# Optimization experiments

Hardware: AMD Instinct MI355X
Metric: run time of the kernel (lower is better)

Reference implementation:

```python
import jax, jax.numpy as jnp
import numpy as np

B, S, C, H, W = 8, 32, 3, 256, 256


def setup_inputs() -> dict:
    key = jax.random.key(0)
    k1, k2 = jax.random.split(key)
    return {
        "input": jax.random.normal(k1, (B, S, C, H, W), dtype=jnp.float32),
        "target": jax.random.normal(k2, (B, C, H, W), dtype=jnp.float32),
    }


def _l2norm(x, axis):
    # F.normalize: x / max(||x||_2, eps)
    return x / jnp.maximum(jnp.linalg.norm(x, axis=axis, keepdims=True), 1e-12)


def _forward(input, target):
    b, s, c, h, w = input.shape
    # target: [B,C,H,W] -> permute(0,1,3,2) -> [B,C,W,H] -> flatten(1,2) -> [B, C*W, H]
    target_f = _l2norm(jnp.transpose(target, (0, 1, 3, 2)).reshape(b, c * w, h), axis=1)
    # input: [B,S,C,H,W] -> permute(0,1,2,4,3) -> [B,S,C,W,H] -> flatten(2,3) -> [B,S,C*W,H]
    input_f = _l2norm(jnp.transpose(input, (0, 1, 2, 4, 3)).reshape(b, s, c * w, h), axis=2)

    def corr_one(xf, wf):
        # xf: [S, C*W, H] as conv batch, wf: [C*W, H] as single-output-channel kernel
        y = jax.lax.conv_general_dilated(
            xf, wf[None], window_strides=(1,), padding=[(h - 1, h - 1)],
            dimension_numbers=("NCH", "OIH", "NCH"))
        return y[:, 0, :h]  # first H shift positions (overlap sizes 1..H)

    corr = jax.vmap(corr_one)(input_f, target_f)  # [B, S, H]
    corr = corr / jnp.arange(1, h + 1, dtype=input.dtype)  # mean over overlap size

    overlap = jnp.argmax(corr, axis=-1)            # [B, S] best overlap per sample
    shift = (h - 1) - overlap                      # rows to shift up by

    # out[b,s,:,r,:] = input[b,s,:,r+shift,:] for r < overlap, else 0
    h_idx = jnp.arange(h)[None, None, :] + shift[:, :, None]  # [B, S, H]
    valid = h_idx < h
    idx = jnp.clip(h_idx, 0, h - 1)[:, :, None, :, None]      # [B,S,1,H,1]
    gathered = jnp.take_along_axis(input, idx, axis=3)
    return jnp.where(valid[:, :, None, :, None], gathered, jnp.zeros((), input.dtype))


def reference(input, target):
    return _forward(input, target)
```

## Files before the change

### kernel.cpp

```cpp
#include <hip/hip_runtime.h>

#define B_ 8
#define S_ 32
#define C_ 3
#define H_ 256
#define W_ 256
#define HW_ (H_*W_)
#define CHW_ (C_*H_*W_)
#define NINROWS (B_*S_*H_)
#define NTGROWS (B_*H_)

typedef __attribute__((ext_vector_type(8))) short bf16x8;
typedef __attribute__((ext_vector_type(4))) float f32x4;

__device__ __forceinline__ ushort f2bf(float x) {
  unsigned u = __float_as_uint(x);
  return (ushort)((u + 0x7FFFu + ((u >> 16) & 1u)) >> 16);
}
__device__ __forceinline__ float bf2f(ushort h) {
  return __uint_as_float(((unsigned)h) << 16);
}

__global__ void ct_norms(const float* __restrict__ input,
                         const float* __restrict__ target,
                         float* __restrict__ nin, float* __restrict__ ntg) {
  int gw = (int)((blockIdx.x * (size_t)blockDim.x + threadIdx.x) >> 6);
  int lane = threadIdx.x & 63;
  const float* base;
  if (gw < NINROWS) {
    int h = gw & (H_-1);
    int bs = gw >> 8;
    base = input + (size_t)bs * CHW_ + (size_t)h * W_;
  } else {
    int r = gw - NINROWS;
    int h = r & (H_-1);
    int b = r >> 8;
    base = target + (size_t)b * CHW_ + (size_t)h * W_;
  }
  float ss = 0.f;
#pragma unroll
  for (int c = 0; c < C_; ++c)
#pragma unroll
    for (int tt = 0; tt < W_/64; ++tt) {
      float v = base[c*HW_ + tt*64 + lane];
      ss = fmaf(v, v, ss);
    }
#pragma unroll
  for (int off = 32; off; off >>= 1) ss += __shfl_xor(ss, off);
  if (lane == 0) {
    float n = fmaxf(sqrtf(ss), 1e-12f);
    if (gw < NINROWS) nin[gw] = n;
    else ntg[gw - NINROWS] = n;
  }
}

__global__ __launch_bounds__(512)
void ct_corr_mfma(const float* __restrict__ input,
                  const float* __restrict__ target,
                  const float* __restrict__ nin,
                  const float* __restrict__ ntg,
                  int* __restrict__ shift_out) {
  __shared__ ushort Ah[8192], Al[8192], Bh[8192], Bl[8192];
  __shared__ float nin_s[256], ntg_s[256], corrS[256];
  __shared__ unsigned long long wkey[4];

  const int bs = blockIdx.x;
  const int b  = bs >> 5;
  const int t  = threadIdx.x;
  const int lane = t & 63;
  const int wid  = t >> 6;
  const int wm   = wid >> 2;
  const int wn   = wid & 3;

  const float* Abase = input  + (size_t)bs * CHW_;
  const float* Tbase = target + (size_t)b  * CHW_;

  if (t < 256) {
    nin_s[t] = nin[bs*256 + t];
    ntg_s[t] = ntg[b*256 + t];
    corrS[t] = 0.f;
  }

  f32x4 acc[8][4];
#pragma unroll
  for (int m = 0; m < 8; ++m)
#pragma unroll
    for (int n = 0; n < 4; ++n) acc[m][n] = (f32x4){0.f, 0.f, 0.f, 0.f};

  float4 pa[4], pb[4];

  auto issue = [&](int kt) {
    const float* Ab = Abase + (size_t)(kt >> 3) * HW_ + (kt & 7) * 32;
    const float* Tb = Tbase + (size_t)(kt >> 3) * HW_ + (kt & 7) * 32;
#pragma unroll
    for (int p = 0; p < 4; ++p) {
      int f   = p * 512 + t;
      int row = (f >> 7) * 16 + ((f >> 1) & 15);
      int kk  = ((f >> 5) & 3) * 8 + (f & 1) * 4;
      pa[p] = *(const float4*)(Ab + (size_t)row * W_ + kk);
      pb[p] = *(const float4*)(Tb + (size_t)row * W_ + kk);
    }
  };

  auto stash = [&]() {
#pragma unroll
    for (int p = 0; p < 4; ++p) {
      int f   = p * 512 + t;
      int idx = (f >> 7) * 512 + ((f >> 5) & 3) * 128 + ((f >> 1) & 15) * 8 + (f & 1) * 4;
      float4 va = pa[p], vb = pb[p];
      ushort4 hv, lv;
      hv.x = f2bf(va.x); lv.x = f2bf(va.x - bf2f(hv.x));
      hv.y = f2bf(va.y); lv.y = f2bf(va.y - bf2f(hv.y));
      hv.z = f2bf(va.z); lv.z = f2bf(va.z - bf2f(hv.z));
      hv.w = f2bf(va.w); lv.w = f2bf(va.w - bf2f(hv.w));
      *(ushort4*)&Ah[idx] = hv;
      *(ushort4*)&Al[idx] = lv;
      hv.x = f2bf(vb.x); lv.x = f2bf(vb.x - bf2f(hv.x));
      hv.y = f2bf(vb.y); lv.y = f2bf(vb.y - bf2f(hv.y));
      hv.z = f2bf(vb.z); lv.z = f2bf(vb.z - bf2f(hv.z));
      hv.w = f2bf(vb.w); lv.w = f2bf(vb.w - bf2f(hv.w));
      *(ushort4*)&Bh[idx] = hv;
      *(ushort4*)&Bl[idx] = lv;
    }
  };

  issue(0);
  for (int kt = 0; kt < 24; ++kt) {
    __syncthreads();
    stash();
    __syncthreads();
    if (kt < 23) issue(kt + 1);

    bf16x8 bh[4], bl[4];
#pragma unroll
    for (int n = 0; n < 4; ++n) {
      int ct = wn * 4 + n;
      bh[n] = *(const bf16x8*)&Bh[ct * 512 + lane * 8];
      bl[n] = *(const bf16x8*)&Bl[ct * 512 + lane * 8];
    }
#pragma unroll
    for (int m = 0; m < 8; ++m) {
      int rt = wm * 8 + m;
      bf16x8 ah = *(const bf16x8*)&Ah[rt * 512 + lane * 8];
      bf16x8 al = *(const bf16x8*)&Al[rt * 512 + lane * 8];
#pragma unroll
      for (int n = 0; n < 4; ++n) {
        acc[m][n] = __builtin_amdgcn_mfma_f32_16x16x32_bf16(ah, bh[n], acc[m][n], 0, 0, 0);
        acc[m][n] = __builtin_amdgcn_mfma_f32_16x16x32_bf16(ah, bl[n], acc[m][n], 0, 0, 0);
        acc[m][n] = __builtin_amdgcn_mfma_f32_16x16x32_bf16(al, bh[n], acc[m][n], 0, 0, 0);
      }
    }
  }

#pragma unroll
  for (int n = 0; n < 4; ++n) {
    int col = wn * 64 + n * 16 + (lane & 15);
    float rc = 1.0f / ntg_s[col];
#pragma unroll
    for (int m = 0; m < 8; ++m) {
      f32x4 a = acc[m][n];
#pragma unroll
      for (int r = 0; r < 4; ++r) {
        int row = wm * 128 + m * 16 + (lane >> 4) * 4 + r;
        int q = col - row;
        if (q >= 0) atomicAdd(&corrS[q], a[r] * (1.0f / nin_s[row]) * rc);
      }
    }
  }
  __syncthreads();

  if (t < 256) {
    int q = 255 - t;
    float v = corrS[q] / (float)(256 - q);
    unsigned u = __float_as_uint(v);
    u = (u & 0x80000000u) ? ~u : (u | 0x80000000u);
    unsigned long long key = ((unsigned long long)u << 32) | (unsigned)q;
#pragma unroll
    for (int off = 32; off; off >>= 1) {
      unsigned long long o = __shfl_xor(key, off);
      if (o > key) key = o;
    }
    if ((t & 63) == 0) wkey[t >> 6] = key;
  }
  __syncthreads();
  if (t == 0) {
    unsigned long long k = wkey[0];
#pragma unroll
    for (int i = 1; i < 4; ++i) if (wkey[i] > k) k = wkey[i];
    shift_out[bs] = (int)(k & 0xFFFFFFFFull);
  }
}

__global__ void ct_gather(const float* __restrict__ input,
                          const int* __restrict__ shift,
                          float* __restrict__ out) {
  size_t idx = (size_t)blockIdx.x * blockDim.x + threadIdx.x;
  int w4 = (int)(idx & 63);
  int h  = (int)((idx >> 6) & 255);
  int sc = (int)(idx >> 14);
  int bs = sc / 3;
  int hh = h + shift[bs];
  float4 v = make_float4(0.f, 0.f, 0.f, 0.f);
  if (hh < H_) v = *(const float4*)(input + ((size_t)sc << 16) + (size_t)hh * W_ + w4*4);
  *(float4*)(out + (idx << 2)) = v;
}

extern "C" void kernel_launch(void* const* d_in, const int* in_sizes, int n_in,
                              void* d_out, int out_size, void* d_ws, size_t ws_size,
                              hipStream_t stream) {
  const float* input  = (const float*)d_in[0];
  const float* target = (const float*)d_in[1];
  float* out  = (float*)d_out;
  float* nin  = (float*)d_ws;
  float* ntg  = nin + NINROWS;
  int*  shift = (int*)(ntg + NTGROWS);

  ct_norms     <<<(NINROWS + NTGROWS) / 4, 256, 0, stream>>>(input, target, nin, ntg);
  ct_corr_mfma <<<B_ * S_, 512, 0, stream>>>(input, target, nin, ntg, shift);
  ct_gather    <<<(B_*S_*C_*H_*W_/4) / 256, 256, 0, stream>>>(input, shift, out);
}
```

Baseline: 190.8 us.

## Fuse row-norm computation into correlation kernel and double-buffer LDS tiles

Drops the separate norm kernel and instead accumulates per-row sums of squares from the tiles already loaded for the MFMA correlation, reducing them in shared memory at the end. This avoids a full extra read of input and target. LDS staging is double-buffered so each tile is converted while the previous one is multiplied, leaving one barrier per iteration. The bf16 hi/lo split now truncates instead of rounding, which slightly changes precision, and the doubled LDS footprint may limit occupancy.

```diff
diff --git a/kernel.cpp b/kernel.cpp
--- a/kernel.cpp
+++ b/kernel.cpp
@@ -7,61 +7,25 @@
 #define W_ 256
 #define HW_ (H_*W_)
 #define CHW_ (C_*H_*W_)
-#define NINROWS (B_*S_*H_)
-#define NTGROWS (B_*H_)
 
 typedef __attribute__((ext_vector_type(8))) short bf16x8;
 typedef __attribute__((ext_vector_type(4))) float f32x4;
 
-__device__ __forceinline__ ushort f2bf(float x) {
-  unsigned u = __float_as_uint(x);
-  return (ushort)((u + 0x7FFFu + ((u >> 16) & 1u)) >> 16);
-}
-__device__ __forceinline__ float bf2f(ushort h) {
-  return __uint_as_float(((unsigned)h) << 16);
-}
-
-__global__ void ct_norms(const float* __restrict__ input,
-                         const float* __restrict__ target,
-                         float* __restrict__ nin, float* __restrict__ ntg) {
-  int gw = (int)((blockIdx.x * (size_t)blockDim.x + threadIdx.x) >> 6);
-  int lane = threadIdx.x & 63;
-  const float* base;
-  if (gw < NINROWS) {
-    int h = gw & (H_-1);
-    int bs = gw >> 8;
-    base = input + (size_t)bs * CHW_ + (size_t)h * W_;
-  } else {
-    int r = gw - NINROWS;
-    int h = r & (H_-1);
-    int b = r >> 8;
-    base = target + (size_t)b * CHW_ + (size_t)h * W_;
-  }
-  float ss = 0.f;
-#pragma unroll
-  for (int c = 0; c < C_; ++c)
-#pragma unroll
-    for (int tt = 0; tt < W_/64; ++tt) {
-      float v = base[c*HW_ + tt*64 + lane];
-      ss = fmaf(v, v, ss);
-    }
-#pragma unroll
-  for (int off = 32; off; off >>= 1) ss += __shfl_xor(ss, off);
-  if (lane == 0) {
-    float n = fmaxf(sqrtf(ss), 1e-12f);
-    if (gw < NINROWS) nin[gw] = n;
-    else ntg[gw - NINROWS] = n;
-  }
+__device__ __forceinline__ void split2(float x, float y, unsigned &hp, unsigned &lp) {
+  unsigned ux = __float_as_uint(x), uy = __float_as_uint(y);
+  unsigned hx = ux & 0xFFFF0000u, hy = uy & 0xFFFF0000u;
+  float lx = x - __uint_as_float(hx);
+  float ly = y - __uint_as_float(hy);
+  hp = (ux >> 16) | hy;
+  lp = (__float_as_uint(lx) >> 16) | (__float_as_uint(ly) & 0xFFFF0000u);
 }
 
 __global__ __launch_bounds__(512)
 void ct_corr_mfma(const float* __restrict__ input,
                   const float* __restrict__ target,
-                  const float* __restrict__ nin,
-                  const float* __restrict__ ntg,
                   int* __restrict__ shift_out) {
-  __shared__ ushort Ah[8192], Al[8192], Bh[8192], Bl[8192];
-  __shared__ float nin_s[256], ntg_s[256], corrS[256];
+  __shared__ ushort Ah[2][8192], Al[2][8192], Bh[2][8192], Bl[2][8192];
+  __shared__ float ninSq[256], ntgSq[256], rnin[256], rntg[256], corrS[256];
   __shared__ unsigned long long wkey[4];
 
   const int bs = blockIdx.x;
@@ -75,11 +39,7 @@
   const float* Abase = input  + (size_t)bs * CHW_;
   const float* Tbase = target + (size_t)b  * CHW_;
 
-  if (t < 256) {
-    nin_s[t] = nin[bs*256 + t];
-    ntg_s[t] = ntg[b*256 + t];
-    corrS[t] = 0.f;
-  }
+  if (t < 256) { ninSq[t] = 0.f; ntgSq[t] = 0.f; corrS[t] = 0.f; }
 
   f32x4 acc[8][4];
 #pragma unroll
@@ -88,6 +48,8 @@
     for (int n = 0; n < 4; ++n) acc[m][n] = (f32x4){0.f, 0.f, 0.f, 0.f};
 
   float4 pa[4], pb[4];
+  float ssA[4] = {0.f, 0.f, 0.f, 0.f};
+  float ssB[4] = {0.f, 0.f, 0.f, 0.f};
 
   auto issue = [&](int kt) {
     const float* Ab = Abase + (size_t)(kt >> 3) * HW_ + (kt & 7) * 32;
@@ -102,47 +64,48 @@
     }
   };
 
-  auto stash = [&]() {
+  auto stash = [&](int sel) {
+    ushort* AhD = Ah[sel]; ushort* AlD = Al[sel];
+    ushort* BhD = Bh[sel]; ushort* BlD = Bl[sel];
 #pragma unroll
     for (int p = 0; p < 4; ++p) {
       int f   = p * 512 + t;
       int idx = (f >> 7) * 512 + ((f >> 5) & 3) * 128 + ((f >> 1) & 15) * 8 + (f & 1) * 4;
       float4 va = pa[p], vb = pb[p];
-      ushort4 hv, lv;
-      hv.x = f2bf(va.x); lv.x = f2bf(va.x - bf2f(hv.x));
-      hv.y = f2bf(va.y); lv.y = f2bf(va.y - bf2f(hv.y));
-      hv.z = f2bf(va.z); lv.z = f2bf(va.z - bf2f(hv.z));
-      hv.w = f2bf(va.w); lv.w = f2bf(va.w - bf2f(hv.w));
-      *(ushort4*)&Ah[idx] = hv;
-      *(ushort4*)&Al[idx] = lv;
-      hv.x = f2bf(vb.x); lv.x = f2bf(vb.x - bf2f(hv.x));
-      hv.y = f2bf(vb.y); lv.y = f2bf(vb.y - bf2f(hv.y));
-      hv.z = f2bf(vb.z); lv.z = f2bf(vb.z - bf2f(hv.z));
-      hv.w = f2bf(vb.w); lv.w = f2bf(vb.w - bf2f(hv.w));
-      *(ushort4*)&Bh[idx] = hv;
-      *(ushort4*)&Bl[idx] = lv;
+      ssA[p] = fmaf(va.x, va.x, fmaf(va.y, va.y, fmaf(va.z, va.z, fmaf(va.w, va.w, ssA[p]))));
+      ssB[p] = fmaf(vb.x, vb.x, fmaf(vb.y, vb.y, fmaf(vb.z, vb.z, fmaf(vb.w, vb.w, ssB[p]))));
+      unsigned h0, l0, h1, l1;
+      split2(va.x, va.y, h0, l0); split2(va.z, va.w, h1, l1);
+      *(uint2*)&AhD[idx] = make_uint2(h0, h1);
+      *(uint2*)&AlD[idx] = make_uint2(l0, l1);
+      split2(vb.x, vb.y, h0, l0); split2(vb.z, vb.w, h1, l1);
+      *(uint2*)&BhD[idx] = make_uint2(h0, h1);
+      *(uint2*)&BlD[idx] = make_uint2(l0, l1);
     }
   };
 
   issue(0);
+  stash(0);
+  issue(1);
+  __syncthreads();
+
   for (int kt = 0; kt < 24; ++kt) {
-    __syncthreads();
-    stash();
-    __syncthreads();
-    if (kt < 23) issue(kt + 1);
+    const int cur = kt & 1, nx = cur ^ 1;
+    const ushort* AhC = Ah[cur]; const ushort* AlC = Al[cur];
+    const ushort* BhC = Bh[cur]; const ushort* BlC = Bl[cur];
 
     bf16x8 bh[4], bl[4];
 #pragma unroll
     for (int n = 0; n < 4; ++n) {
       int ct = wn * 4 + n;
-      bh[n] = *(const bf16x8*)&Bh[ct * 512 + lane * 8];
-      bl[n] = *(const bf16x8*)&Bl[ct * 512 + lane * 8];
+      bh[n] = *(const bf16x8*)&BhC[ct * 512 + lane * 8];
+      bl[n] = *(const bf16x8*)&BlC[ct * 512 + lane * 8];
     }
 #pragma unroll
     for (int m = 0; m < 8; ++m) {
       int rt = wm * 8 + m;
-      bf16x8 ah = *(const bf16x8*)&Ah[rt * 512 + lane * 8];
-      bf16x8 al = *(const bf16x8*)&Al[rt * 512 + lane * 8];
+      bf16x8 ah = *(const bf16x8*)&AhC[rt * 512 + lane * 8];
+      bf16x8 al = *(const bf16x8*)&AlC[rt * 512 + lane * 8];
 #pragma unroll
       for (int n = 0; n < 4; ++n) {
         acc[m][n] = __builtin_amdgcn_mfma_f32_16x16x32_bf16(ah, bh[n], acc[m][n], 0, 0, 0);
@@ -150,12 +113,28 @@
         acc[m][n] = __builtin_amdgcn_mfma_f32_16x16x32_bf16(al, bh[n], acc[m][n], 0, 0, 0);
       }
     }
+    if (kt < 23) stash(nx);
+    if (kt < 22) issue(kt + 2);
+    __syncthreads();
   }
+
+#pragma unroll
+  for (int p = 0; p < 4; ++p) {
+    int row = (p * 4 + (t >> 7)) * 16 + ((t >> 1) & 15);
+    atomicAdd(&ninSq[row], ssA[p]);
+    atomicAdd(&ntgSq[row], ssB[p]);
+  }
+  __syncthreads();
+  if (t < 256) {
+    rnin[t] = 1.0f / fmaxf(sqrtf(ninSq[t]), 1e-12f);
+    rntg[t] = 1.0f / fmaxf(sqrtf(ntgSq[t]), 1e-12f);
+  }
+  __syncthreads();
 
 #pragma unroll
   for (int n = 0; n < 4; ++n) {
     int col = wn * 64 + n * 16 + (lane & 15);
-    float rc = 1.0f / ntg_s[col];
+    float rc = rntg[col];
 #pragma unroll
     for (int m = 0; m < 8; ++m) {
       f32x4 a = acc[m][n];
@@ -163,7 +142,7 @@
       for (int r = 0; r < 4; ++r) {
         int row = wm * 128 + m * 16 + (lane >> 4) * 4 + r;
         int q = col - row;
-        if (q >= 0) atomicAdd(&corrS[q], a[r] * (1.0f / nin_s[row]) * rc);
+        if (q >= 0) atomicAdd(&corrS[q], a[r] * rnin[row] * rc);
       }
     }
   }
@@ -211,11 +190,8 @@
   const float* input  = (const float*)d_in[0];
   const float* target = (const float*)d_in[1];
   float* out  = (float*)d_out;
-  float* nin  = (float*)d_ws;
-  float* ntg  = nin + NINROWS;
-  int*  shift = (int*)(ntg + NTGROWS);
+  int*  shift = (int*)d_ws;
 
-  ct_norms     <<<(NINROWS + NTGROWS) / 4, 256, 0, stream>>>(input, target, nin, ntg);
-  ct_corr_mfma <<<B_ * S_, 512, 0, stream>>>(input, target, nin, ntg, shift);
+  ct_corr_mfma <<<B_ * S_, 512, 0, stream>>>(input, target, shift);
   ct_gather    <<<(B_*S_*C_*H_*W_/4) / 256, 256, 0, stream>>>(input, shift, out);
 }
```

Result: faster. 167.4 us (-12.2%).
